# Kernel tuning notes

Hardware: AMD Instinct MI355X
Metric: run time of the kernel (lower is better)

## Reference

```python
import jax, jax.numpy as jnp
import numpy as np

B, S, D = 8, 2048, 64
H = 128


def setup_inputs() -> dict:
    key = jax.random.key(0)
    k = jax.random.split(key, 5)
    X = jax.random.normal(k[0], (B, S, D), dtype=jnp.float32)
    Wi = jax.random.normal(k[1], (H, D), dtype=jnp.float32)          # init_layer weight, std=1
    bi = jax.random.normal(k[2], (H,), dtype=jnp.float32)            # init_layer bias, std=1
    Wa = jax.random.normal(k[3], (H * H, D + 1), dtype=jnp.float32) / jnp.sqrt(H)  # vf_A, std=1/sqrt(H)
    Wb = jax.random.normal(k[4], (H, D + 1), dtype=jnp.float32)      # vf_B, std=1
    return {"X": X, "Wi": Wi, "bi": bi, "Wa": Wa, "Wb": Wb}


def reference(X, Wi, bi, Wa, Wb):
    b, s, d = X.shape
    dt = 1.0 / (s - 1)
    # inp: time channel (constant dt) concatenated with scaled input -> [b, s, d+1]
    inp = jnp.concatenate([jnp.full((b, s, 1), dt, dtype=X.dtype), X * dt], axis=-1)
    y0 = X[:, 0] @ Wi.T + bi                       # [b, H]
    Bs = jnp.einsum('bsk,hk->bsh', inp[:, 1:], Wb)  # [b, s-1, H]

    def step(y, xs):
        inp_t, b_t = xs                            # [b, d+1], [b, H]
        A = (inp_t @ Wa.T).reshape(b, H, H)        # per-step transition matrix
        y_new = y + jnp.einsum('bij,bj->bi', A, y) + b_t
        return y_new, y_new

    xs = (jnp.swapaxes(inp[:, 1:], 0, 1), jnp.swapaxes(Bs, 0, 1))  # time-major
    _, ys_rest = jax.lax.scan(step, y0, xs)        # [s-1, b, H]
    ys = jnp.concatenate([y0[:, None, :], jnp.swapaxes(ys_rest, 0, 1)], axis=1)
    return ys
```

## Files before the change

kernel.cpp:

```cpp
#include <hip/hip_runtime.h>
#include <hip/hip_fp16.h>


typedef _Float16 h8 __attribute__((ext_vector_type(8)));
typedef float v4f __attribute__((ext_vector_type(4)));
typedef unsigned int uint;

constexpr int B_ = 8, S_ = 2048, D_ = 64, H_ = 128;
constexpr int T_ = S_ - 1;
constexpr int KD = D_ + 1;
constexpr float DTC = 1.0f / 2047.0f;
constexpr int L_ = 8;
constexpr int LSH = 3;
constexpr int NC = 256;

__global__ __launch_bounds__(256) void k_prep(const float* __restrict__ Wa,
                                              _Float16* __restrict__ Wa16B,
                                              float* __restrict__ Wa0,
                                              const float* __restrict__ X,
                                              _Float16* __restrict__ Xs16,
                                              const float* __restrict__ Wb,
                                              float* __restrict__ Bs,
                                              const float* __restrict__ Wi,
                                              const float* __restrict__ bi,
                                              float* __restrict__ out,
                                              float* __restrict__ yb) {
  __shared__ float wb_s[H_ * KD];
  __shared__ float xs[16][D_ + 4];
  int bx = blockIdx.x, tid = threadIdx.x;
  if (bx < 4096) {
    int idx = bx * 256 + tid;
    int r = idx >> 6, kk = idx & 63;
    int rt = r >> 4, n = r & 15;
    int kb = kk >> 5, q = (kk >> 3) & 3, jj = kk & 7;
    float v = Wa[(size_t)r * KD + 1 + kk];
    Wa16B[((((size_t)rt * 2 + kb) * 4 + q) * 16 + n) * 8 + jj] = (_Float16)v;
    if (kk == 0) Wa0[r] = Wa[(size_t)r * KD];
  } else if (bx < 8190) {
    int idx = (bx - 4096) * 256 + tid;
    if (idx < B_ * T_ * 64) {
      int bt = idx >> 6, d = idx & 63;
      int b = bt / T_, s = bt - b * T_;
      Xs16[(size_t)bt * 64 + d] = (_Float16)(X[((size_t)b * S_ + s + 1) * D_ + d] * DTC);
    }
  } else if (bx < 9214) {
    int bt0 = (bx - 8190) * 16;
    for (int i2 = tid; i2 < H_ * KD; i2 += 256) wb_s[i2] = Wb[i2];
    for (int i2 = tid; i2 < 16 * D_; i2 += 256) {
      int sl = i2 >> 6, d = i2 & 63;
      int btg = bt0 + sl;
      float v = 0.f;
      if (btg < B_ * T_) {
        int b = btg / T_, s = btg - b * T_;
        v = X[((size_t)b * S_ + s + 1) * D_ + d] * DTC;
      }
      xs[sl][d] = v;
    }
    __syncthreads();
    int h = tid & 127, sh = tid >> 7;
    const float* wrow = &wb_s[h * KD];
    for (int u = 0; u < 8; u++) {
      int sl = sh * 8 + u;
      int btg = bt0 + sl;
      if (btg >= B_ * T_) break;
      float acc = wrow[0] * DTC;
#pragma unroll 8
      for (int d = 0; d < D_; d++) acc += xs[sl][d] * wrow[1 + d];
      Bs[(size_t)btg * H_ + h] = acc;
    }
  } else {
    int b = bx - 9214;
    if (tid < D_) xs[0][tid] = X[(size_t)b * S_ * D_ + tid];
    __syncthreads();
    if (tid < H_) {
      float acc = bi[tid];
      const float* wr = Wi + tid * D_;
#pragma unroll 8
      for (int d = 0; d < D_; d++) acc += xs[0][d] * wr[d];
      out[(size_t)b * S_ * H_ + tid] = acc;
      yb[(size_t)(b * NC + 0) * H_ + tid] = acc;
    }
  }
}

__global__ __launch_bounds__(256) void k_amat(const _Float16* __restrict__ Xs16,
                                              const _Float16* __restrict__ Wa16B,
                                              const float* __restrict__ Wa0,
                                              _Float16* __restrict__ A_sl,
                                              int c0, int scShift) {
  __shared__ _Float16 sb[32 * 528];
  int tid = threadIdx.x;
  int w = tid >> 6, lane = tid & 63;
  int n = lane & 15, q = lane >> 4;
  int rowbase = blockIdx.x * 32;
  int SCm = ((1 << scShift) << LSH) - 1;

  h8 af[2][2];
#pragma unroll
  for (int mi = 0; mi < 2; mi++) {
    int sidx = rowbase + mi * 16 + n;
    int b = sidx >> (scShift + LSH);
    int rem = sidx & SCm;
    int cc = rem >> LSH, l = rem & (L_ - 1);
    int s = (c0 + cc) * L_ + l;
    if (s >= T_) s = T_ - 1;
    size_t btg = (size_t)b * T_ + s;
#pragma unroll
    for (int kb = 0; kb < 2; kb++)
      af[mi][kb] = *(const h8*)(Xs16 + btg * 64 + kb * 32 + q * 8);
  }

  v4f acc[2][8];
#pragma unroll
  for (int nj = 0; nj < 8; nj++) {
    int ct_g = blockIdx.y * 32 + w * 8 + nj;
    float binit = DTC * Wa0[ct_g * 16 + n];
    h8 bf0 = *(const h8*)(Wa16B + ((((size_t)ct_g * 2 + 0) * 4 + q) * 16 + n) * 8);
    h8 bf1 = *(const h8*)(Wa16B + ((((size_t)ct_g * 2 + 1) * 4 + q) * 16 + n) * 8);
#pragma unroll
    for (int mi = 0; mi < 2; mi++) {
      v4f a;
      a[0] = binit; a[1] = binit; a[2] = binit; a[3] = binit;
      a = __builtin_amdgcn_mfma_f32_16x16x32_f16(af[mi][0], bf0, a, 0, 0, 0);
      a = __builtin_amdgcn_mfma_f32_16x16x32_f16(af[mi][1], bf1, a, 0, 0, 0);
      acc[mi][nj] = a;
    }
  }
#pragma unroll
  for (int mi = 0; mi < 2; mi++)
#pragma unroll
    for (int nj = 0; nj < 8; nj++)
#pragma unroll
      for (int reg = 0; reg < 4; reg++)
        sb[(mi * 16 + q * 4 + reg) * 528 + w * 128 + ((nj * 16 + n) ^ (q * 16))] =
            (_Float16)acc[mi][nj][reg];
  __syncthreads();
#pragma unroll
  for (int it = 0; it < 8; it++) {
    int idx = tid + it * 256;
    int t = idx >> 6, u4 = idx & 63;
    int qt = (t >> 2) & 3;
    uint4 val = *(const uint4*)&sb[t * 528 + ((u4 * 8) ^ (qt * 16))];
    *(uint4*)(A_sl + (size_t)(rowbase + t) * 16384 + blockIdx.y * 512 + u4 * 8) = val;
  }
}

__device__ __forceinline__ void chunkmap_body(const _Float16* __restrict__ A_sl,
                                              const float* __restrict__ Bs,
                                              _Float16* __restrict__ Mr,
                                              float* __restrict__ vch,
                                              int c0, int scShift, int chunk, int tid,
                                              _Float16* Dt, float* v32) {
  int w = tid >> 6, lane = tid & 63;
  int n = lane & 15, q = lane >> 4;
  int SC = 1 << scShift;
  int b = chunk >> scShift;
  int cc = chunk & (SC - 1);
  int c = c0 + cc;
  int sbase = c * L_;
  int nsteps = min(L_, T_ - sbase);
  const _Float16* Abase = A_sl + (size_t)chunk * L_ * 16384;
  size_t btb = (size_t)b * T_ + sbase;

#pragma unroll
  for (int it = 0; it < 8; it++) {
    int idx = tid + it * 256;
    int rowl = idx & 127, c8 = (idx >> 7) * 8;
    uint4 pk = *(const uint4*)(Abase + rowl * 128 + c8);
    const _Float16* hp = (const _Float16*)&pk;
#pragma unroll
    for (int cx = 0; cx < 8; cx++) Dt[(c8 + cx) * 136 + rowl] = hp[cx];
  }
  if (tid < 128) v32[tid] = Bs[btb * 128 + tid];
  h8 idE, idO;
#pragma unroll
  for (int jj = 0; jj < 8; jj++) {
    idE[jj] = (_Float16)((q * 8 + jj == n) ? 1.f : 0.f);
    idO[jj] = (_Float16)((q * 8 + jj == 16 + n) ? 1.f : 0.f);
  }
  __syncthreads();

  v4f acc[2][8];
#pragma unroll
  for (int mi = 0; mi < 2; mi++) {
    int row0 = (2 * w + mi) * 16 + q * 4;
#pragma unroll
    for (int nj = 0; nj < 8; nj++) {
      int col = nj * 16 + n;
      union { uint2 u; _Float16 h[4]; } m2;
      m2.u = *(const uint2*)&Dt[col * 136 + row0];
#pragma unroll
      for (int reg = 0; reg < 4; reg++) acc[mi][nj][reg] = (float)m2.h[reg];
    }
  }

  int r0 = 2 * w * 16 + n, r1 = r0 + 16;
  h8 afA[2][4], afB[2][4];

#define LOADA(dst, l)                                                                \
  {                                                                                  \
    const _Float16* Ag = Abase + (size_t)(l) * 16384;                                \
    _Pragma("unroll")                                                                \
    for (int mi = 0; mi < 2; mi++)                                                   \
      _Pragma("unroll")                                                              \
      for (int kb = 0; kb < 4; kb++)                                                 \
        dst[mi][kb] = *(const h8*)(Ag + ((2 * w + mi) * 16 + n) * 128 + kb * 32 + q * 8); \
  }

#define STEPQ(af, l)                                                                 \
  {                                                                                  \
    _Pragma("unroll")                                                                \
    for (int nj = 0; nj < 8; nj++) {                                                 \
      h8 bfr[4];                                                                     \
      _Pragma("unroll")                                                              \
      for (int kb = 0; kb < 4; kb++)                                                 \
        bfr[kb] = *(const h8*)&Dt[(nj * 16 + n) * 136 + kb * 32 + q * 8];            \
      _Pragma("unroll")                                                              \
      for (int mi = 0; mi < 2; mi++) {                                               \
        _Pragma("unroll")                                                            \
        for (int kb = 0; kb < 4; kb++)                                               \
          acc[mi][nj] = __builtin_amdgcn_mfma_f32_16x16x32_f16(af[mi][kb], bfr[kb], acc[mi][nj], 0, 0, 0); \
        acc[mi][nj] = __builtin_amdgcn_mfma_f32_16x16x32_f16(                        \
            af[mi][nj >> 1], (nj & 1) ? idO : idE, acc[mi][nj], 0, 0, 0);            \
      }                                                                              \
    }                                                                                \
    float dv0 = 0.f, dv1 = 0.f;                                                      \
    _Pragma("unroll")                                                                \
    for (int kb = 0; kb < 4; kb++) {                                                 \
      float4 p0 = *(const float4*)&v32[kb * 32 + q * 8];                             \
      float4 p1 = *(const float4*)&v32[kb * 32 + q * 8 + 4];                         \
      float vk[8] = {p0.x, p0.y, p0.z, p0.w, p1.x, p1.y, p1.z, p1.w};                \
      _Pragma("unroll")                                                              \
      for (int jj = 0; jj < 8; jj++) {                                               \
        dv0 += (float)af[0][kb][jj] * vk[jj];                                        \
        dv1 += (float)af[1][kb][jj] * vk[jj];                                        \
      }                                                                              \
    }                                                                                \
    dv0 += __shfl_xor(dv0, 16); dv0 += __shfl_xor(dv0, 32);                          \
    dv1 += __shfl_xor(dv1, 16); dv1 += __shfl_xor(dv1, 32);                          \
    float vold0 = v32[r0], vold1 = v32[r1];                                          \
    float bs0 = 0.f, bs1 = 0.f;                                                      \
    if (q == 0) {                                                                    \
      bs0 = Bs[(btb + (l)) * 128 + r0];                                              \
      bs1 = Bs[(btb + (l)) * 128 + r1];                                              \
    }                                                                                \
    __syncthreads();                                                                 \
    _Pragma("unroll")                                                                \
    for (int mi = 0; mi < 2; mi++) {                                                 \
      int row0 = (2 * w + mi) * 16 + q * 4;                                          \
      _Pragma("unroll")                                                              \
      for (int nj = 0; nj < 8; nj++) {                                               \
        int col = nj * 16 + n;                                                       \
        union { _Float16 h[4]; uint2 u; } pk;                                        \
        _Pragma("unroll")                                                            \
        for (int reg = 0; reg < 4; reg++) pk.h[reg] = (_Float16)acc[mi][nj][reg];    \
        *(uint2*)&Dt[col * 136 + row0] = pk.u;                                       \
      }                                                                              \
    }                                                                                \
    if (q == 0) {                                                                    \
      v32[r0] = vold0 + dv0 + bs0;                                                   \
      v32[r1] = vold1 + dv1 + bs1;                                                   \
    }                                                                                \
    __syncthreads();                                                                 \
  }

  LOADA(afA, 1);
  for (int l = 1; l < nsteps; l += 2) {
    if (l + 1 < nsteps) LOADA(afB, l + 1);
    STEPQ(afA, l);
    if (l + 2 < nsteps) LOADA(afA, l + 2);
    if (l + 1 < nsteps) STEPQ(afB, l + 1);
  }
#undef LOADA
#undef STEPQ

#pragma unroll
  for (int mi = 0; mi < 2; mi++) {
    int row0 = (2 * w + mi) * 16 + q * 4;
#pragma unroll
    for (int nj = 0; nj < 8; nj++) {
      int col = nj * 16 + n;
#pragma unroll
      for (int reg = 0; reg < 4; reg++)
        Dt[(row0 + reg) * 136 + col] = (_Float16)acc[mi][nj][reg];
    }
  }
  __syncthreads();
  _Float16* og = Mr + (size_t)chunk * 16384;
#pragma unroll
  for (int it = 0; it < 8; it++) {
    int idx = tid + it * 256;
    int rowl = idx >> 4, ch = idx & 15;
    uint4 val = *(const uint4*)&Dt[rowl * 136 + ch * 8];
    *(uint4*)(og + rowl * 128 + ch * 8) = val;
  }
  if (tid < 128) vch[(size_t)chunk * 128 + tid] = v32[tid];
}

__device__ __forceinline__ void comp4_body(const _Float16* __restrict__ in_map,
                                           const float* __restrict__ in_v,
                                           _Float16* __restrict__ out_map,
                                           float* __restrict__ out_v,
                                           int outIdx, int tid,
                                           _Float16* Dt, float* v32) {
  int w = tid >> 6, lane = tid & 63;
  int n = lane & 15, q = lane >> 4;
  size_t nbase = (size_t)outIdx * 4;

  const _Float16* P0 = in_map + nbase * 16384;
#pragma unroll
  for (int it = 0; it < 8; it++) {
    int idx = tid + it * 256;
    int rowl = idx & 127, c8 = (idx >> 7) * 8;
    uint4 pk = *(const uint4*)(P0 + rowl * 128 + c8);
    const _Float16* hp = (const _Float16*)&pk;
#pragma unroll
    for (int cx = 0; cx < 8; cx++) Dt[(c8 + cx) * 136 + rowl] = hp[cx];
  }
  if (tid < 128) v32[tid] = in_v[nbase * 128 + tid];
  h8 idE, idO;
#pragma unroll
  for (int jj = 0; jj < 8; jj++) {
    idE[jj] = (_Float16)((q * 8 + jj == n) ? 1.f : 0.f);
    idO[jj] = (_Float16)((q * 8 + jj == 16 + n) ? 1.f : 0.f);
  }
  __syncthreads();

  v4f acc[2][8];
#pragma unroll
  for (int mi = 0; mi < 2; mi++) {
    int row0 = (2 * w + mi) * 16 + q * 4;
#pragma unroll
    for (int nj = 0; nj < 8; nj++) {
      int col = nj * 16 + n;
      union { uint2 u; _Float16 h[4]; } m2;
      m2.u = *(const uint2*)&Dt[col * 136 + row0];
#pragma unroll
      for (int reg = 0; reg < 4; reg++) acc[mi][nj][reg] = (float)m2.h[reg];
    }
  }

  int r0 = 2 * w * 16 + n, r1 = r0 + 16;
  for (int j = 1; j < 4; j++) {
    const _Float16* Pj = in_map + (nbase + j) * 16384;
    h8 af[2][4];
#pragma unroll
    for (int mi = 0; mi < 2; mi++)
#pragma unroll
      for (int kb = 0; kb < 4; kb++)
        af[mi][kb] = *(const h8*)(Pj + ((2 * w + mi) * 16 + n) * 128 + kb * 32 + q * 8);
#pragma unroll
    for (int nj = 0; nj < 8; nj++) {
      h8 bfr[4];
#pragma unroll
      for (int kb = 0; kb < 4; kb++)
        bfr[kb] = *(const h8*)&Dt[(nj * 16 + n) * 136 + kb * 32 + q * 8];
#pragma unroll
      for (int mi = 0; mi < 2; mi++) {
#pragma unroll
        for (int kb = 0; kb < 4; kb++)
          acc[mi][nj] = __builtin_amdgcn_mfma_f32_16x16x32_f16(af[mi][kb], bfr[kb], acc[mi][nj], 0, 0, 0);
        acc[mi][nj] = __builtin_amdgcn_mfma_f32_16x16x32_f16(
            af[mi][nj >> 1], (nj & 1) ? idO : idE, acc[mi][nj], 0, 0, 0);
      }
    }
    float dv0 = 0.f, dv1 = 0.f;
#pragma unroll
    for (int kb = 0; kb < 4; kb++) {
      float4 p0 = *(const float4*)&v32[kb * 32 + q * 8];
      float4 p1 = *(const float4*)&v32[kb * 32 + q * 8 + 4];
      float vk[8] = {p0.x, p0.y, p0.z, p0.w, p1.x, p1.y, p1.z, p1.w};
#pragma unroll
      for (int jj = 0; jj < 8; jj++) {
        dv0 += (float)af[0][kb][jj] * vk[jj];
        dv1 += (float)af[1][kb][jj] * vk[jj];
      }
    }
    dv0 += __shfl_xor(dv0, 16); dv0 += __shfl_xor(dv0, 32);
    dv1 += __shfl_xor(dv1, 16); dv1 += __shfl_xor(dv1, 32);
    float vold0 = v32[r0], vold1 = v32[r1];
    float vj0 = 0.f, vj1 = 0.f;
    if (q == 0) {
      vj0 = in_v[(nbase + j) * 128 + r0];
      vj1 = in_v[(nbase + j) * 128 + r1];
    }
    __syncthreads();
#pragma unroll
    for (int mi = 0; mi < 2; mi++) {
      int row0 = (2 * w + mi) * 16 + q * 4;
#pragma unroll
      for (int nj = 0; nj < 8; nj++) {
        int col = nj * 16 + n;
        union { _Float16 h[4]; uint2 u; } pk;
#pragma unroll
        for (int reg = 0; reg < 4; reg++) pk.h[reg] = (_Float16)acc[mi][nj][reg];
        *(uint2*)&Dt[col * 136 + row0] = pk.u;
      }
    }
    if (q == 0) {
      v32[r0] = vold0 + dv0 + vj0;
      v32[r1] = vold1 + dv1 + vj1;
    }
    __syncthreads();
  }
#pragma unroll
  for (int mi = 0; mi < 2; mi++) {
    int row0 = (2 * w + mi) * 16 + q * 4;
#pragma unroll
    for (int nj = 0; nj < 8; nj++) {
      int col = nj * 16 + n;
#pragma unroll
      for (int reg = 0; reg < 4; reg++)
        Dt[(row0 + reg) * 136 + col] = (_Float16)acc[mi][nj][reg];
    }
  }
  __syncthreads();
  _Float16* og = out_map + (size_t)outIdx * 16384;
#pragma unroll
  for (int it = 0; it < 8; it++) {
    int idx = tid + it * 256;
    int rowl = idx >> 4, ch = idx & 15;
    uint4 val = *(const uint4*)&Dt[rowl * 136 + ch * 8];
    *(uint4*)(og + rowl * 128 + ch * 8) = val;
  }
  if (tid < 128) out_v[(size_t)outIdx * 128 + tid] = v32[tid];
}

__device__ __forceinline__ void chainsuper_body(const _Float16* __restrict__ Sr,
                                                const float* __restrict__ sv,
                                                float* __restrict__ yb,
                                                int c0, int scShift, int b, int tid,
                                                float* ybuf, float* red) {
  int NS = 1 << (scShift - 2);
  int i = tid >> 1, hh = tid & 1;
  if (tid < 128) ybuf[tid] = yb[(size_t)(b * NC + c0) * 128 + tid];
  __syncthreads();

  uint4 arA[8], arB[8];
  float svA, svB;

#define LOADS(ar, svv, s)                                                            \
  {                                                                                  \
    const uint4* p = (const uint4*)(Sr + (size_t)(b * NS + (s)) * 16384 + i * 128 + hh * 64); \
    _Pragma("unroll")                                                                \
    for (int u = 0; u < 8; u++) ar[u] = p[u];                                        \
    svv = sv[(size_t)(b * NS + (s)) * 128 + i];                                      \
  }

#define STEPS(ar, svv, s)                                                            \
  {                                                                                  \
    float pt = 0.f;                                                                  \
    _Pragma("unroll")                                                                \
    for (int u = 0; u < 8; u++) {                                                    \
      union { uint4 v; _Float16 h[8]; } wv; wv.v = ar[u];                            \
      _Pragma("unroll")                                                              \
      for (int k = 0; k < 8; k++) pt += (float)wv.h[k] * ybuf[hh * 64 + u * 8 + k];  \
    }                                                                                \
    if (hh) red[i] = pt;                                                             \
    __syncthreads();                                                                 \
    if (!hh) {                                                                       \
      float yn = ybuf[i] + pt + red[i] + svv;                                        \
      int cg = c0 + 4 * ((s) + 1);                                                   \
      if (cg < NC) yb[(size_t)(b * NC + cg) * 128 + i] = yn;                         \
      ybuf[i] = yn;                                                                  \
    }                                                                                \
    __syncthreads();                                                                 \
  }

  LOADS(arA, svA, 0);
  int s = 0;
  for (; s + 1 < NS; s += 2) {
    LOADS(arB, svB, s + 1);
    STEPS(arA, svA, s);
    if (s + 2 < NS) LOADS(arA, svA, s + 2);
    STEPS(arB, svB, s + 1);
  }
  if (s < NS) STEPS(arA, svA, s);
#undef LOADS
#undef STEPS
}

__device__ __forceinline__ void emit_body(const _Float16* __restrict__ A_sl,
                                          const float* __restrict__ Bs,
                                          const _Float16* __restrict__ Mr,
                                          const float* __restrict__ vch,
                                          const float* __restrict__ yb,
                                          float* __restrict__ out,
                                          int tid, int b, int c, int kpre, int cbase,
                                          int nst, size_t node0, size_t sidx0, size_t btb,
                                          uint4* arA, float bsA, uint4* arP, float vvP,
                                          float* ybuf, float* red) {
  int i = tid >> 1, hh = tid & 1;
  if (tid < 128) ybuf[tid] = yb[(size_t)(b * NC + cbase) * 128 + tid];
  __syncthreads();

  for (int j = 0; j < kpre; j++) {
    uint4 ar[8];
    float vv;
    if (j == 0) {
#pragma unroll
      for (int u = 0; u < 8; u++) ar[u] = arP[u];
      vv = vvP;
    } else {
      const uint4* p = (const uint4*)(Mr + (node0 + j) * 16384 + i * 128 + hh * 64);
#pragma unroll
      for (int u = 0; u < 8; u++) ar[u] = p[u];
      vv = vch[(node0 + j) * 128 + i];
    }
    float pt = 0.f;
#pragma unroll
    for (int u = 0; u < 8; u++) {
      union { uint4 v; _Float16 h[8]; } wv; wv.v = ar[u];
#pragma unroll
      for (int k = 0; k < 8; k++) pt += (float)wv.h[k] * ybuf[hh * 64 + u * 8 + k];
    }
    if (hh) red[i] = pt;
    __syncthreads();
    if (!hh) {
      float yn = ybuf[i] + pt + red[i] + vv;
      ybuf[i] = yn;
    }
    __syncthreads();
  }

  uint4 arB[8];
  float bsB;

#define LOADR(ar, bsv, l)                                                            \
  {                                                                                  \
    const uint4* p = (const uint4*)(A_sl + (sidx0 + (l)) * 16384 + i * 128 + hh * 64); \
    _Pragma("unroll")                                                                \
    for (int u = 0; u < 8; u++) ar[u] = p[u];                                        \
    bsv = Bs[(btb + (l)) * 128 + i];                                                 \
  }

#define STEPE(ar, bsv, l)                                                            \
  {                                                                                  \
    float pt = 0.f;                                                                  \
    _Pragma("unroll")                                                                \
    for (int u = 0; u < 8; u++) {                                                    \
      union { uint4 v; _Float16 h[8]; } wv; wv.v = ar[u];                            \
      _Pragma("unroll")                                                              \
      for (int k = 0; k < 8; k++) pt += (float)wv.h[k] * ybuf[hh * 64 + u * 8 + k];  \
    }                                                                                \
    if (hh) red[i] = pt;                                                             \
    __syncthreads();                                                                 \
    if (!hh) {                                                                       \
      float yn = ybuf[i] + pt + red[i] + bsv;                                        \
      out[((size_t)b * S_ + (size_t)(c * L_ + (l) + 1)) * 128 + i] = yn;             \
      ybuf[i] = yn;                                                                  \
    }                                                                                \
    __syncthreads();                                                                 \
  }

  for (int l = 0; l < nst; l += 2) {
    if (l + 1 < nst) LOADR(arB, bsB, l + 1);
    STEPE(arA, bsA, l);
    if (l + 2 < nst) LOADR(arA, bsA, l + 2);
    if (l + 1 < nst) STEPE(arB, bsB, l + 1);
  }
#undef LOADR
#undef STEPE
}

__global__ __launch_bounds__(256) void k_chunkmap(const _Float16* __restrict__ A_sl,
                                                  const float* __restrict__ Bs,
                                                  _Float16* __restrict__ Mr,
                                                  float* __restrict__ vch,
                                                  int c0, int scShift) {
  __shared__ _Float16 Dt[128 * 136];
  __shared__ float v32[128];
  chunkmap_body(A_sl, Bs, Mr, vch, c0, scShift, blockIdx.x, threadIdx.x, Dt, v32);
}

__global__ __launch_bounds__(256) void k_comp4(const _Float16* __restrict__ in_map,
                                               const float* __restrict__ in_v,
                                               _Float16* __restrict__ out_map,
                                               float* __restrict__ out_v) {
  __shared__ _Float16 Dt[128 * 136];
  __shared__ float v32[128];
  comp4_body(in_map, in_v, out_map, out_v, blockIdx.x, threadIdx.x, Dt, v32);
}

__global__ __launch_bounds__(256) void k_chainsuper(const _Float16* __restrict__ Sr,
                                                    const float* __restrict__ sv,
                                                    float* __restrict__ yb,
                                                    int c0, int scShift) {
  __shared__ float ybuf[128];
  __shared__ float red[128];
  chainsuper_body(Sr, sv, yb, c0, scShift, blockIdx.x, threadIdx.x, ybuf, red);
}

__global__ __launch_bounds__(256) void k_emit(const _Float16* __restrict__ A_sl,
                                              const float* __restrict__ Bs,
                                              const _Float16* __restrict__ Mr,
                                              const float* __restrict__ vch,
                                              const float* __restrict__ yb,
                                              float* __restrict__ out,
                                              int c0, int scShift) {
  __shared__ float ybuf[128];
  __shared__ float red[128];
  int tid = threadIdx.x;
  int SC = 1 << scShift;
  int b = blockIdx.x >> scShift;
  int cc = blockIdx.x & (SC - 1);
  int c = c0 + cc;
  int i = tid >> 1, hh = tid & 1;
  int kpre = cc & 3;
  int cbase = c - kpre;
  size_t node0 = ((size_t)b << scShift) + (cc & ~3);
  int nst = min(L_, T_ - c * L_);
  size_t sidx0 = (size_t)blockIdx.x * L_;
  size_t btb = (size_t)b * T_ + c * L_;
  uint4 arA[8], arP[8];
  float bsA, vvP = 0.f;
  {
    const uint4* p = (const uint4*)(A_sl + sidx0 * 16384 + i * 128 + hh * 64);
#pragma unroll
    for (int u = 0; u < 8; u++) arA[u] = p[u];
    bsA = Bs[btb * 128 + i];
  }
  if (kpre > 0) {
    const uint4* p2 = (const uint4*)(Mr + node0 * 16384 + i * 128 + hh * 64);
#pragma unroll
    for (int u = 0; u < 8; u++) arP[u] = p2[u];
    vvP = vch[node0 * 128 + i];
  }
  emit_body(A_sl, Bs, Mr, vch, yb, out, tid, b, c, kpre, cbase, nst, node0, sidx0, btb,
            arA, bsA, arP, vvP, ybuf, red);
}

__global__ __launch_bounds__(256) void k_seq(const float* __restrict__ X,
                                             const float* __restrict__ Wa,
                                             const float* __restrict__ Wb,
                                             float* __restrict__ out) {
  int b = blockIdx.x, tid = threadIdx.x;
  int i = tid >> 1, hh = tid & 1;
  __shared__ float y[H_], red[H_], xs[D_], bts[H_];
  if (tid < H_) y[tid] = out[(size_t)b * S_ * H_ + tid];
  __syncthreads();
  for (int t = 1; t < S_; t++) {
    if (tid < D_) xs[tid] = X[((size_t)b * S_ + t) * D_ + tid] * DTC;
    __syncthreads();
    if (tid < H_) {
      const float* wr = Wb + tid * KD;
      float acc = wr[0] * DTC;
#pragma unroll 8
      for (int d = 0; d < D_; d++) acc += xs[d] * wr[1 + d];
      bts[tid] = acc;
    }
    float part = 0.f;
    const float* yhalf = &y[hh * 64];
    for (int j = 0; j < 64; j++) {
      const float* wr = Wa + ((size_t)(i * H_) + hh * 64 + j) * KD;
      float a = wr[0] * DTC;
#pragma unroll 8
      for (int d = 0; d < D_; d++) a += xs[d] * wr[1 + d];
      part += a * yhalf[j];
    }
    if (hh) red[i] = part;
    __syncthreads();
    if (!hh) {
      float yn = y[i] + part + red[i] + bts[i];
      out[((size_t)b * S_ + t) * H_ + i] = yn;
      y[i] = yn;
    }
    __syncthreads();
  }
}

__global__ __launch_bounds__(128) void k_y0f(const float* __restrict__ X,
                                             const float* __restrict__ Wi,
                                             const float* __restrict__ bi,
                                             float* __restrict__ out) {
  int b = blockIdx.x, h = threadIdx.x;
  __shared__ float xs[D_];
  if (h < D_) xs[h] = X[(size_t)b * S_ * D_ + h];
  __syncthreads();
  float acc = bi[h];
  const float* wr = Wi + h * D_;
#pragma unroll 8
  for (int d = 0; d < D_; d++) acc += xs[d] * wr[d];
  out[(size_t)b * S_ * H_ + h] = acc;
}

extern "C" void kernel_launch(void* const* d_in, const int* in_sizes, int n_in,
                              void* d_out, int out_size, void* d_ws, size_t ws_size,
                              hipStream_t stream) {
  (void)in_sizes; (void)n_in; (void)out_size;
  const float* X  = (const float*)d_in[0];
  const float* Wi = (const float*)d_in[1];
  const float* bi = (const float*)d_in[2];
  const float* Wa = (const float*)d_in[3];
  const float* Wb = (const float*)d_in[4];
  float* out = (float*)d_out;
  char* ws = (char*)d_ws;

  size_t off = 0;
  auto alloc = [&](size_t bytes) { size_t o = off; off = (off + bytes + 255) & ~(size_t)255; return o; };
  size_t oBs  = alloc((size_t)B_ * T_ * 128 * 4);
  size_t oYb  = alloc((size_t)B_ * NC * 128 * 4);
  size_t oWaB = alloc((size_t)64 * 16384 * 2);
  size_t oWa0 = alloc((size_t)16384 * 4);
  size_t oXs  = alloc((size_t)B_ * T_ * 64 * 2);
  size_t fixed = off;

  const size_t APC  = (size_t)B_ * L_ * 16384 * 2;
  const size_t MRPC = (size_t)B_ * 16384 * 2;
  const size_t VCPC = (size_t)B_ * 128 * 4;
  const size_t SRPC = (size_t)B_ * 16384 * 2 / 4;
  const size_t SVPC = (size_t)B_ * 128;
  const size_t PER_SC = APC + MRPC + VCPC + SRPC + SVPC + 5 * 256;

  int SC = 0;
  if (ws_size > fixed) {
    size_t avail = ws_size - fixed;
    SC = 128;
    while (SC >= 4 && (size_t)SC * PER_SC > avail) SC >>= 1;
    if (SC < 4) SC = 0;
  }
  if (SC < 4) {
    k_y0f<<<B_, 128, 0, stream>>>(X, Wi, bi, out);
    k_seq<<<B_, 256, 0, stream>>>(X, Wa, Wb, out);
    return;
  }
  int scShift = __builtin_ctz(SC);

  size_t oMr = alloc((size_t)SC * MRPC);
  size_t oVc = alloc((size_t)SC * VCPC);
  size_t oSr = alloc((size_t)SC * SRPC);
  size_t oSv = alloc((size_t)SC * SVPC);
  size_t oA  = alloc((size_t)SC * APC);

  float*    Bs    = (float*)(ws + oBs);
  float*    yb    = (float*)(ws + oYb);
  _Float16* Wa16B = (_Float16*)(ws + oWaB);
  float*    Wa0   = (float*)(ws + oWa0);
  _Float16* Xs16  = (_Float16*)(ws + oXs);
  _Float16* Mr    = (_Float16*)(ws + oMr);
  float*    vch   = (float*)(ws + oVc);
  _Float16* Sr    = (_Float16*)(ws + oSr);
  float*    sv    = (float*)(ws + oSv);
  _Float16* A_sl  = (_Float16*)(ws + oA);

  k_prep<<<9222, 256, 0, stream>>>(Wa, Wa16B, Wa0, X, Xs16, Wb, Bs, Wi, bi, out, yb);

  int nslices = NC / SC;
  int chunks = B_ * SC;
  int amat_gx = (B_ * SC * L_) / 32;
  for (int si = 0; si < nslices; si++) {
    int c0 = si * SC;
    k_amat<<<dim3(amat_gx, 32), 256, 0, stream>>>(Xs16, Wa16B, Wa0, A_sl, c0, scShift);
    k_chunkmap<<<chunks, 256, 0, stream>>>(A_sl, Bs, Mr, vch, c0, scShift);
    k_comp4<<<chunks / 4, 256, 0, stream>>>(Mr, vch, Sr, sv);
    k_chainsuper<<<B_, 256, 0, stream>>>(Sr, sv, yb, c0, scShift);
    k_emit<<<chunks, 256, 0, stream>>>(A_sl, Bs, Mr, vch, yb, out, c0, scShift);
  }
}
```

Measured before the change: 607.0 us.

## Fuse chunkmap+comp4 into one kernel and fold superchain scan into emit

Merges the per-chunk map kernel and the 4-way composition kernel into a single k_smap kernel, where each block builds four chunk maps and then composes them. It also removes the serial 8-block k_chainsuper launch: each emit block now redundantly replays the superchunk prefix from the slice start up to its own group. The last group writes the carry-in for the next slice. This cuts three launches per slice and the low-occupancy serial chain kernel. In exchange, emit blocks do redundant matvec work, up to NS steps for the later chunks, and k_smap runs 4x fewer blocks serially over its chunks.

```diff
diff --git a/kernel.cpp b/kernel.cpp
--- a/kernel.cpp
+++ b/kernel.cpp
@@ -426,20 +426,58 @@
   if (tid < 128) out_v[(size_t)outIdx * 128 + tid] = v32[tid];
 }
 
-__device__ __forceinline__ void chainsuper_body(const _Float16* __restrict__ Sr,
-                                                const float* __restrict__ sv,
-                                                float* __restrict__ yb,
-                                                int c0, int scShift, int b, int tid,
-                                                float* ybuf, float* red) {
-  int NS = 1 << (scShift - 2);
+__global__ __launch_bounds__(256) void k_smap(const _Float16* __restrict__ A_sl,
+                                              const float* __restrict__ Bs,
+                                              _Float16* __restrict__ Mr,
+                                              float* __restrict__ vch,
+                                              _Float16* __restrict__ Sr,
+                                              float* __restrict__ sv,
+                                              int c0, int scShift) {
+  __shared__ _Float16 Dt[128 * 136];
+  __shared__ float v32[128];
+  int tid = threadIdx.x;
+  int gb = blockIdx.x;
+  for (int cI = 0; cI < 4; cI++) {
+    chunkmap_body(A_sl, Bs, Mr, vch, c0, scShift, gb * 4 + cI, tid, Dt, v32);
+    __syncthreads();
+  }
+  __threadfence_block();
+  __syncthreads();
+  comp4_body(Mr, vch, Sr, sv, gb, tid, Dt, v32);
+}
+
+__global__ __launch_bounds__(256) void k_emit(const _Float16* __restrict__ A_sl,
+                                              const float* __restrict__ Bs,
+                                              const _Float16* __restrict__ Mr,
+                                              const float* __restrict__ vch,
+                                              const _Float16* __restrict__ Sr,
+                                              const float* __restrict__ sv,
+                                              float* __restrict__ yb,
+                                              float* __restrict__ out,
+                                              int c0, int scShift) {
+  __shared__ float ybuf[128];
+  __shared__ float red[128];
+  int tid = threadIdx.x;
+  int SC = 1 << scShift;
+  int NS = SC >> 2;
+  int b = blockIdx.x >> scShift;
+  int cc = blockIdx.x & (SC - 1);
+  int c = c0 + cc;
   int i = tid >> 1, hh = tid & 1;
+  int kpre = cc & 3;
+  int gsup = cc >> 2;
+  size_t node0 = ((size_t)b << scShift) + (cc & ~3);
+  int nst = min(L_, T_ - c * L_);
+  size_t sidx0 = (size_t)blockIdx.x * L_;
+  size_t btb = (size_t)b * T_ + c * L_;
+
   if (tid < 128) ybuf[tid] = yb[(size_t)(b * NC + c0) * 128 + tid];
   __syncthreads();
 
-  uint4 arA[8], arB[8];
+  uint4 sA[8], sB[8];
   float svA, svB;
 
-#define LOADS(ar, svv, s)                                                            \
+#define SLOAD(ar, svv, s)                                                            \
   {                                                                                  \
     const uint4* p = (const uint4*)(Sr + (size_t)(b * NS + (s)) * 16384 + i * 128 + hh * 64); \
     _Pragma("unroll")                                                                \
@@ -447,7 +485,7 @@
     svv = sv[(size_t)(b * NS + (s)) * 128 + i];                                      \
   }
 
-#define STEPS(ar, svv, s)                                                            \
+#define SSTEP(ar, svv)                                                               \
   {                                                                                  \
     float pt = 0.f;                                                                  \
     _Pragma("unroll")                                                                \
@@ -458,55 +496,45 @@
     }                                                                                \
     if (hh) red[i] = pt;                                                             \
     __syncthreads();                                                                 \
-    if (!hh) {                                                                       \
-      float yn = ybuf[i] + pt + red[i] + svv;                                        \
-      int cg = c0 + 4 * ((s) + 1);                                                   \
-      if (cg < NC) yb[(size_t)(b * NC + cg) * 128 + i] = yn;                         \
-      ybuf[i] = yn;                                                                  \
-    }                                                                                \
+    if (!hh) ybuf[i] = ybuf[i] + pt + red[i] + svv;                                  \
     __syncthreads();                                                                 \
   }
 
-  LOADS(arA, svA, 0);
-  int s = 0;
-  for (; s + 1 < NS; s += 2) {
-    LOADS(arB, svB, s + 1);
-    STEPS(arA, svA, s);
-    if (s + 2 < NS) LOADS(arA, svA, s + 2);
-    STEPS(arB, svB, s + 1);
-  }
-  if (s < NS) STEPS(arA, svA, s);
-#undef LOADS
-#undef STEPS
-}
-
-__device__ __forceinline__ void emit_body(const _Float16* __restrict__ A_sl,
-                                          const float* __restrict__ Bs,
-                                          const _Float16* __restrict__ Mr,
-                                          const float* __restrict__ vch,
-                                          const float* __restrict__ yb,
-                                          float* __restrict__ out,
-                                          int tid, int b, int c, int kpre, int cbase,
-                                          int nst, size_t node0, size_t sidx0, size_t btb,
-                                          uint4* arA, float bsA, uint4* arP, float vvP,
-                                          float* ybuf, float* red) {
-  int i = tid >> 1, hh = tid & 1;
-  if (tid < 128) ybuf[tid] = yb[(size_t)(b * NC + cbase) * 128 + tid];
-  __syncthreads();
+  if (gsup > 0) {
+    SLOAD(sA, svA, 0);
+    int s = 0;
+    for (; s + 1 < gsup; s += 2) {
+      SLOAD(sB, svB, s + 1);
+      SSTEP(sA, svA);
+      if (s + 2 < gsup) SLOAD(sA, svA, s + 2);
+      SSTEP(sB, svB);
+    }
+    if (s < gsup) SSTEP(sA, svA);
+  }
+
+  if (cc == SC - 4 && c0 + SC < NC) {
+    SLOAD(sA, svA, NS - 1);
+    float pt = 0.f;
+#pragma unroll
+    for (int u = 0; u < 8; u++) {
+      union { uint4 v; _Float16 h[8]; } wv; wv.v = sA[u];
+#pragma unroll
+      for (int k = 0; k < 8; k++) pt += (float)wv.h[k] * ybuf[hh * 64 + u * 8 + k];
+    }
+    if (hh) red[i] = pt;
+    __syncthreads();
+    if (!hh) yb[(size_t)(b * NC + c0 + SC) * 128 + i] = ybuf[i] + pt + red[i] + svA;
+    __syncthreads();
+  }
+#undef SLOAD
+#undef SSTEP
 
   for (int j = 0; j < kpre; j++) {
     uint4 ar[8];
-    float vv;
-    if (j == 0) {
-#pragma unroll
-      for (int u = 0; u < 8; u++) ar[u] = arP[u];
-      vv = vvP;
-    } else {
-      const uint4* p = (const uint4*)(Mr + (node0 + j) * 16384 + i * 128 + hh * 64);
-#pragma unroll
-      for (int u = 0; u < 8; u++) ar[u] = p[u];
-      vv = vch[(node0 + j) * 128 + i];
-    }
+    const uint4* p = (const uint4*)(Mr + (node0 + j) * 16384 + i * 128 + hh * 64);
+#pragma unroll
+    for (int u = 0; u < 8; u++) ar[u] = p[u];
+    float vv = vch[(node0 + j) * 128 + i];
     float pt = 0.f;
 #pragma unroll
     for (int u = 0; u < 8; u++) {
@@ -523,8 +551,8 @@
     __syncthreads();
   }
 
-  uint4 arB[8];
-  float bsB;
+  uint4 arA[8], arB[8];
+  float bsA, bsB;
 
 #define LOADR(ar, bsv, l)                                                            \
   {                                                                                  \
@@ -553,6 +581,7 @@
     __syncthreads();                                                                 \
   }
 
+  LOADR(arA, bsA, 0);
   for (int l = 0; l < nst; l += 2) {
     if (l + 1 < nst) LOADR(arB, bsB, l + 1);
     STEPE(arA, bsA, l);
@@ -561,73 +590,6 @@
   }
 #undef LOADR
 #undef STEPE
-}
-
-__global__ __launch_bounds__(256) void k_chunkmap(const _Float16* __restrict__ A_sl,
-                                                  const float* __restrict__ Bs,
-                                                  _Float16* __restrict__ Mr,
-                                                  float* __restrict__ vch,
-                                                  int c0, int scShift) {
-  __shared__ _Float16 Dt[128 * 136];
-  __shared__ float v32[128];
-  chunkmap_body(A_sl, Bs, Mr, vch, c0, scShift, blockIdx.x, threadIdx.x, Dt, v32);
-}
-
-__global__ __launch_bounds__(256) void k_comp4(const _Float16* __restrict__ in_map,
-                                               const float* __restrict__ in_v,
-                                               _Float16* __restrict__ out_map,
-                                               float* __restrict__ out_v) {
-  __shared__ _Float16 Dt[128 * 136];
-  __shared__ float v32[128];
-  comp4_body(in_map, in_v, out_map, out_v, blockIdx.x, threadIdx.x, Dt, v32);
-}
-
-__global__ __launch_bounds__(256) void k_chainsuper(const _Float16* __restrict__ Sr,
-                                                    const float* __restrict__ sv,
-                                                    float* __restrict__ yb,
-                                                    int c0, int scShift) {
-  __shared__ float ybuf[128];
-  __shared__ float red[128];
-  chainsuper_body(Sr, sv, yb, c0, scShift, blockIdx.x, threadIdx.x, ybuf, red);
-}
-
-__global__ __launch_bounds__(256) void k_emit(const _Float16* __restrict__ A_sl,
-                                              const float* __restrict__ Bs,
-                                              const _Float16* __restrict__ Mr,
-                                              const float* __restrict__ vch,
-                                              const float* __restrict__ yb,
-                                              float* __restrict__ out,
-                                              int c0, int scShift) {
-  __shared__ float ybuf[128];
-  __shared__ float red[128];
-  int tid = threadIdx.x;
-  int SC = 1 << scShift;
-  int b = blockIdx.x >> scShift;
-  int cc = blockIdx.x & (SC - 1);
-  int c = c0 + cc;
-  int i = tid >> 1, hh = tid & 1;
-  int kpre = cc & 3;
-  int cbase = c - kpre;
-  size_t node0 = ((size_t)b << scShift) + (cc & ~3);
-  int nst = min(L_, T_ - c * L_);
-  size_t sidx0 = (size_t)blockIdx.x * L_;
-  size_t btb = (size_t)b * T_ + c * L_;
-  uint4 arA[8], arP[8];
-  float bsA, vvP = 0.f;
-  {
-    const uint4* p = (const uint4*)(A_sl + sidx0 * 16384 + i * 128 + hh * 64);
-#pragma unroll
-    for (int u = 0; u < 8; u++) arA[u] = p[u];
-    bsA = Bs[btb * 128 + i];
-  }
-  if (kpre > 0) {
-    const uint4* p2 = (const uint4*)(Mr + node0 * 16384 + i * 128 + hh * 64);
-#pragma unroll
-    for (int u = 0; u < 8; u++) arP[u] = p2[u];
-    vvP = vch[node0 * 128 + i];
-  }
-  emit_body(A_sl, Bs, Mr, vch, yb, out, tid, b, c, kpre, cbase, nst, node0, sidx0, btb,
-            arA, bsA, arP, vvP, ybuf, red);
 }
 
 __global__ __launch_bounds__(256) void k_seq(const float* __restrict__ X,
@@ -751,9 +713,7 @@
   for (int si = 0; si < nslices; si++) {
     int c0 = si * SC;
     k_amat<<<dim3(amat_gx, 32), 256, 0, stream>>>(Xs16, Wa16B, Wa0, A_sl, c0, scShift);
-    k_chunkmap<<<chunks, 256, 0, stream>>>(A_sl, Bs, Mr, vch, c0, scShift);
-    k_comp4<<<chunks / 4, 256, 0, stream>>>(Mr, vch, Sr, sv);
-    k_chainsuper<<<B_, 256, 0, stream>>>(Sr, sv, yb, c0, scShift);
-    k_emit<<<chunks, 256, 0, stream>>>(A_sl, Bs, Mr, vch, yb, out, c0, scShift);
-  }
-}
+    k_smap<<<chunks / 4, 256, 0, stream>>>(A_sl, Bs, Mr, vch, Sr, sv, c0, scShift);
+    k_emit<<<chunks, 256, 0, stream>>>(A_sl, Bs, Mr, vch, Sr, sv, yb, out, c0, scShift);
+  }
+}
```

Result: slower. 783.3 us (+29.1%).

## Double-buffer shared state to drop per-step barriers; shuffle-reduce partial dots

Applied to the files above, without the earlier changes.

Ping-pong buffers replace the single shared Dt/v32 tiles in the chunk-map and compose kernels, so the write-before-overwrite barrier in each step can go, leaving one barrier per step. In the chain and emit kernels the two-half dot product is now combined with a lane shuffle instead of a shared scratch array and an extra barrier, and the y state is double-buffered. The super-chunk count cap drops from 128 to 64. Shared memory per block roughly doubles for the map kernels, which can lower occupancy, and the smaller chunk count changes how work is split across stages.

```diff
diff --git a/kernel.cpp b/kernel.cpp
--- a/kernel.cpp
+++ b/kernel.cpp
@@ -13,6 +13,7 @@
 constexpr int L_ = 8;
 constexpr int LSH = 3;
 constexpr int NC = 256;
+constexpr int DTS = 128 * 136;
 
 __global__ __launch_bounds__(256) void k_prep(const float* __restrict__ Wa,
                                               _Float16* __restrict__ Wa16B,
@@ -209,12 +210,17 @@
 
 #define STEPQ(af, l)                                                                 \
   {                                                                                  \
+    int cu_ = ((l) - 1) & 1;                                                         \
+    const _Float16* Dr = Dt + cu_ * DTS;                                             \
+    _Float16* Dw = Dt + (cu_ ^ 1) * DTS;                                             \
+    const float* vr = v32 + cu_ * 128;                                               \
+    float* vw = v32 + (cu_ ^ 1) * 128;                                               \
     _Pragma("unroll")                                                                \
     for (int nj = 0; nj < 8; nj++) {                                                 \
       h8 bfr[4];                                                                     \
       _Pragma("unroll")                                                              \
       for (int kb = 0; kb < 4; kb++)                                                 \
-        bfr[kb] = *(const h8*)&Dt[(nj * 16 + n) * 136 + kb * 32 + q * 8];            \
+        bfr[kb] = *(const h8*)&Dr[(nj * 16 + n) * 136 + kb * 32 + q * 8];            \
       _Pragma("unroll")                                                              \
       for (int mi = 0; mi < 2; mi++) {                                               \
         _Pragma("unroll")                                                            \
@@ -227,8 +233,8 @@
     float dv0 = 0.f, dv1 = 0.f;                                                      \
     _Pragma("unroll")                                                                \
     for (int kb = 0; kb < 4; kb++) {                                                 \
-      float4 p0 = *(const float4*)&v32[kb * 32 + q * 8];                             \
-      float4 p1 = *(const float4*)&v32[kb * 32 + q * 8 + 4];                         \
+      float4 p0 = *(const float4*)&vr[kb * 32 + q * 8];                              \
+      float4 p1 = *(const float4*)&vr[kb * 32 + q * 8 + 4];                          \
       float vk[8] = {p0.x, p0.y, p0.z, p0.w, p1.x, p1.y, p1.z, p1.w};                \
       _Pragma("unroll")                                                              \
       for (int jj = 0; jj < 8; jj++) {                                               \
@@ -238,13 +244,12 @@
     }                                                                                \
     dv0 += __shfl_xor(dv0, 16); dv0 += __shfl_xor(dv0, 32);                          \
     dv1 += __shfl_xor(dv1, 16); dv1 += __shfl_xor(dv1, 32);                          \
-    float vold0 = v32[r0], vold1 = v32[r1];                                          \
+    float vold0 = vr[r0], vold1 = vr[r1];                                            \
     float bs0 = 0.f, bs1 = 0.f;                                                      \
     if (q == 0) {                                                                    \
       bs0 = Bs[(btb + (l)) * 128 + r0];                                              \
       bs1 = Bs[(btb + (l)) * 128 + r1];                                              \
     }                                                                                \
-    __syncthreads();                                                                 \
     _Pragma("unroll")                                                                \
     for (int mi = 0; mi < 2; mi++) {                                                 \
       int row0 = (2 * w + mi) * 16 + q * 4;                                          \
@@ -254,12 +259,12 @@
         union { _Float16 h[4]; uint2 u; } pk;                                        \
         _Pragma("unroll")                                                            \
         for (int reg = 0; reg < 4; reg++) pk.h[reg] = (_Float16)acc[mi][nj][reg];    \
-        *(uint2*)&Dt[col * 136 + row0] = pk.u;                                       \
+        *(uint2*)&Dw[col * 136 + row0] = pk.u;                                       \
       }                                                                              \
     }                                                                                \
     if (q == 0) {                                                                    \
-      v32[r0] = vold0 + dv0 + bs0;                                                   \
-      v32[r1] = vold1 + dv1 + bs1;                                                   \
+      vw[r0] = vold0 + dv0 + bs0;                                                    \
+      vw[r1] = vold1 + dv1 + bs1;                                                    \
     }                                                                                \
     __syncthreads();                                                                 \
   }
@@ -294,7 +299,7 @@
     uint4 val = *(const uint4*)&Dt[rowl * 136 + ch * 8];
     *(uint4*)(og + rowl * 128 + ch * 8) = val;
   }
-  if (tid < 128) vch[(size_t)chunk * 128 + tid] = v32[tid];
+  if (tid < 128) vch[(size_t)chunk * 128 + tid] = v32[((nsteps - 1) & 1) * 128 + tid];
 }
 
 __device__ __forceinline__ void comp4_body(const _Float16* __restrict__ in_map,
@@ -342,6 +347,11 @@
 
   int r0 = 2 * w * 16 + n, r1 = r0 + 16;
   for (int j = 1; j < 4; j++) {
+    int cu_ = (j - 1) & 1;
+    const _Float16* Dr = Dt + cu_ * DTS;
+    _Float16* Dw = Dt + (cu_ ^ 1) * DTS;
+    const float* vr = v32 + cu_ * 128;
+    float* vw = v32 + (cu_ ^ 1) * 128;
     const _Float16* Pj = in_map + (nbase + j) * 16384;
     h8 af[2][4];
 #pragma unroll
@@ -354,7 +364,7 @@
       h8 bfr[4];
 #pragma unroll
       for (int kb = 0; kb < 4; kb++)
-        bfr[kb] = *(const h8*)&Dt[(nj * 16 + n) * 136 + kb * 32 + q * 8];
+        bfr[kb] = *(const h8*)&Dr[(nj * 16 + n) * 136 + kb * 32 + q * 8];
 #pragma unroll
       for (int mi = 0; mi < 2; mi++) {
 #pragma unroll
@@ -367,8 +377,8 @@
     float dv0 = 0.f, dv1 = 0.f;
 #pragma unroll
     for (int kb = 0; kb < 4; kb++) {
-      float4 p0 = *(const float4*)&v32[kb * 32 + q * 8];
-      float4 p1 = *(const float4*)&v32[kb * 32 + q * 8 + 4];
+      float4 p0 = *(const float4*)&vr[kb * 32 + q * 8];
+      float4 p1 = *(const float4*)&vr[kb * 32 + q * 8 + 4];
       float vk[8] = {p0.x, p0.y, p0.z, p0.w, p1.x, p1.y, p1.z, p1.w};
 #pragma unroll
       for (int jj = 0; jj < 8; jj++) {
@@ -378,13 +388,12 @@
     }
     dv0 += __shfl_xor(dv0, 16); dv0 += __shfl_xor(dv0, 32);
     dv1 += __shfl_xor(dv1, 16); dv1 += __shfl_xor(dv1, 32);
-    float vold0 = v32[r0], vold1 = v32[r1];
+    float vold0 = vr[r0], vold1 = vr[r1];
     float vj0 = 0.f, vj1 = 0.f;
     if (q == 0) {
       vj0 = in_v[(nbase + j) * 128 + r0];
       vj1 = in_v[(nbase + j) * 128 + r1];
     }
-    __syncthreads();
 #pragma unroll
     for (int mi = 0; mi < 2; mi++) {
       int row0 = (2 * w + mi) * 16 + q * 4;
@@ -394,12 +403,12 @@
         union { _Float16 h[4]; uint2 u; } pk;
 #pragma unroll
         for (int reg = 0; reg < 4; reg++) pk.h[reg] = (_Float16)acc[mi][nj][reg];
-        *(uint2*)&Dt[col * 136 + row0] = pk.u;
+        *(uint2*)&Dw[col * 136 + row0] = pk.u;
       }
     }
     if (q == 0) {
-      v32[r0] = vold0 + dv0 + vj0;
-      v32[r1] = vold1 + dv1 + vj1;
+      vw[r0] = vold0 + dv0 + vj0;
+      vw[r1] = vold1 + dv1 + vj1;
     }
     __syncthreads();
   }
@@ -423,18 +432,19 @@
     uint4 val = *(const uint4*)&Dt[rowl * 136 + ch * 8];
     *(uint4*)(og + rowl * 128 + ch * 8) = val;
   }
-  if (tid < 128) out_v[(size_t)outIdx * 128 + tid] = v32[tid];
+  if (tid < 128) out_v[(size_t)outIdx * 128 + tid] = v32[128 + tid];
 }
 
 __device__ __forceinline__ void chainsuper_body(const _Float16* __restrict__ Sr,
                                                 const float* __restrict__ sv,
                                                 float* __restrict__ yb,
                                                 int c0, int scShift, int b, int tid,
-                                                float* ybuf, float* red) {
+                                                float* ybuf2) {
   int NS = 1 << (scShift - 2);
   int i = tid >> 1, hh = tid & 1;
-  if (tid < 128) ybuf[tid] = yb[(size_t)(b * NC + c0) * 128 + tid];
-  __syncthreads();
+  if (tid < 128) ybuf2[tid] = yb[(size_t)(b * NC + c0) * 128 + tid];
+  __syncthreads();
+  int cur = 0;
 
   uint4 arA[8], arB[8];
   float svA, svB;
@@ -449,21 +459,25 @@
 
 #define STEPS(ar, svv, s)                                                            \
   {                                                                                  \
+    const float* yr = ybuf2 + cur * 128;                                             \
+    float* yw = ybuf2 + (cur ^ 1) * 128;                                             \
     float pt = 0.f;                                                                  \
     _Pragma("unroll")                                                                \
     for (int u = 0; u < 8; u++) {                                                    \
       union { uint4 v; _Float16 h[8]; } wv; wv.v = ar[u];                            \
       _Pragma("unroll")                                                              \
-      for (int k = 0; k < 8; k++) pt += (float)wv.h[k] * ybuf[hh * 64 + u * 8 + k];  \
-    }                                                                                \
-    if (hh) red[i] = pt;                                                             \
-    __syncthreads();                                                                 \
+      for (int k = 0; k < 8; k++) pt += (float)wv.h[k] * yr[hh * 64 + u * 8 + k];    \
+    }                                                                                \
+    float ptO = __shfl_xor(pt, 1);                                                   \
     if (!hh) {                                                                       \
-      float yn = ybuf[i] + pt + red[i] + svv;                                        \
+      float yn = yr[i] + pt;                                                         \
+      yn = yn + ptO;                                                                 \
+      yn = yn + svv;                                                                 \
       int cg = c0 + 4 * ((s) + 1);                                                   \
       if (cg < NC) yb[(size_t)(b * NC + cg) * 128 + i] = yn;                         \
-      ybuf[i] = yn;                                                                  \
-    }                                                                                \
+      yw[i] = yn;                                                                    \
+    }                                                                                \
+    cur ^= 1;                                                                        \
     __syncthreads();                                                                 \
   }
 
@@ -489,10 +503,11 @@
                                           int tid, int b, int c, int kpre, int cbase,
                                           int nst, size_t node0, size_t sidx0, size_t btb,
                                           uint4* arA, float bsA, uint4* arP, float vvP,
-                                          float* ybuf, float* red) {
+                                          float* ybuf2) {
   int i = tid >> 1, hh = tid & 1;
-  if (tid < 128) ybuf[tid] = yb[(size_t)(b * NC + cbase) * 128 + tid];
-  __syncthreads();
+  if (tid < 128) ybuf2[tid] = yb[(size_t)(b * NC + cbase) * 128 + tid];
+  __syncthreads();
+  int cur = 0;
 
   for (int j = 0; j < kpre; j++) {
     uint4 ar[8];
@@ -507,19 +522,23 @@
       for (int u = 0; u < 8; u++) ar[u] = p[u];
       vv = vch[(node0 + j) * 128 + i];
     }
+    const float* yr = ybuf2 + cur * 128;
+    float* yw = ybuf2 + (cur ^ 1) * 128;
     float pt = 0.f;
 #pragma unroll
     for (int u = 0; u < 8; u++) {
       union { uint4 v; _Float16 h[8]; } wv; wv.v = ar[u];
 #pragma unroll
-      for (int k = 0; k < 8; k++) pt += (float)wv.h[k] * ybuf[hh * 64 + u * 8 + k];
-    }
-    if (hh) red[i] = pt;
-    __syncthreads();
+      for (int k = 0; k < 8; k++) pt += (float)wv.h[k] * yr[hh * 64 + u * 8 + k];
+    }
+    float ptO = __shfl_xor(pt, 1);
     if (!hh) {
-      float yn = ybuf[i] + pt + red[i] + vv;
-      ybuf[i] = yn;
-    }
+      float yn = yr[i] + pt;
+      yn = yn + ptO;
+      yn = yn + vv;
+      yw[i] = yn;
+    }
+    cur ^= 1;
     __syncthreads();
   }
 
@@ -536,20 +555,24 @@
 
 #define STEPE(ar, bsv, l)                                                            \
   {                                                                                  \
+    const float* yr = ybuf2 + cur * 128;                                             \
+    float* yw = ybuf2 + (cur ^ 1) * 128;                                             \
     float pt = 0.f;                                                                  \
     _Pragma("unroll")                                                                \
     for (int u = 0; u < 8; u++) {                                                    \
       union { uint4 v; _Float16 h[8]; } wv; wv.v = ar[u];                            \
       _Pragma("unroll")                                                              \
-      for (int k = 0; k < 8; k++) pt += (float)wv.h[k] * ybuf[hh * 64 + u * 8 + k];  \
-    }                                                                                \
-    if (hh) red[i] = pt;                                                             \
-    __syncthreads();                                                                 \
+      for (int k = 0; k < 8; k++) pt += (float)wv.h[k] * yr[hh * 64 + u * 8 + k];    \
+    }                                                                                \
+    float ptO = __shfl_xor(pt, 1);                                                   \
     if (!hh) {                                                                       \
-      float yn = ybuf[i] + pt + red[i] + bsv;                                        \
+      float yn = yr[i] + pt;                                                         \
+      yn = yn + ptO;                                                                 \
+      yn = yn + bsv;                                                                 \
       out[((size_t)b * S_ + (size_t)(c * L_ + (l) + 1)) * 128 + i] = yn;             \
-      ybuf[i] = yn;                                                                  \
-    }                                                                                \
+      yw[i] = yn;                                                                    \
+    }                                                                                \
+    cur ^= 1;                                                                        \
     __syncthreads();                                                                 \
   }
 
@@ -568,8 +591,8 @@
                                                   _Float16* __restrict__ Mr,
                                                   float* __restrict__ vch,
                                                   int c0, int scShift) {
-  __shared__ _Float16 Dt[128 * 136];
-  __shared__ float v32[128];
+  __shared__ _Float16 Dt[2 * DTS];
+  __shared__ float v32[2 * 128];
   chunkmap_body(A_sl, Bs, Mr, vch, c0, scShift, blockIdx.x, threadIdx.x, Dt, v32);
 }
 
@@ -577,8 +600,8 @@
                                                const float* __restrict__ in_v,
                                                _Float16* __restrict__ out_map,
                                                float* __restrict__ out_v) {
-  __shared__ _Float16 Dt[128 * 136];
-  __shared__ float v32[128];
+  __shared__ _Float16 Dt[2 * DTS];
+  __shared__ float v32[2 * 128];
   comp4_body(in_map, in_v, out_map, out_v, blockIdx.x, threadIdx.x, Dt, v32);
 }
 
@@ -586,9 +609,8 @@
                                                     const float* __restrict__ sv,
                                                     float* __restrict__ yb,
                                                     int c0, int scShift) {
-  __shared__ float ybuf[128];
-  __shared__ float red[128];
-  chainsuper_body(Sr, sv, yb, c0, scShift, blockIdx.x, threadIdx.x, ybuf, red);
+  __shared__ float ybuf2[2 * 128];
+  chainsuper_body(Sr, sv, yb, c0, scShift, blockIdx.x, threadIdx.x, ybuf2);
 }
 
 __global__ __launch_bounds__(256) void k_emit(const _Float16* __restrict__ A_sl,
@@ -598,8 +620,7 @@
                                               const float* __restrict__ yb,
                                               float* __restrict__ out,
                                               int c0, int scShift) {
-  __shared__ float ybuf[128];
-  __shared__ float red[128];
+  __shared__ float ybuf2[2 * 128];
   int tid = threadIdx.x;
   int SC = 1 << scShift;
   int b = blockIdx.x >> scShift;
@@ -627,7 +648,7 @@
     vvP = vch[node0 * 128 + i];
   }
   emit_body(A_sl, Bs, Mr, vch, yb, out, tid, b, c, kpre, cbase, nst, node0, sidx0, btb,
-            arA, bsA, arP, vvP, ybuf, red);
+            arA, bsA, arP, vvP, ybuf2);
 }
 
 __global__ __launch_bounds__(256) void k_seq(const float* __restrict__ X,
@@ -715,7 +736,7 @@
   int SC = 0;
   if (ws_size > fixed) {
     size_t avail = ws_size - fixed;
-    SC = 128;
+    SC = 64;
     while (SC >= 4 && (size_t)SC * PER_SC > avail) SC >>= 1;
     if (SC < 4) SC = 0;
   }
```

After: 608.1 us. About the same (+0.2%).
